# Optimization experiments

Hardware: AMD Instinct MI355X
Metric: run time of the kernel (lower is better)

Reference implementation:

```python
import jax, jax.numpy as jnp
import numpy as np

N = 50000          # num_nodes
E = 800000         # num_edges (avg degree 16)
HID = 128          # hidden_dim
NH = 8             # num_heads
HD = 16            # head_dim
FFN = 512          # ffn_dim
EPS = 1e-5


def setup_inputs() -> dict:
    key = jax.random.key(0)
    ks = jax.random.split(key, 12)
    s = 0.02
    d = {}
    d["x"] = jax.random.normal(ks[0], (N, HID), jnp.float32)
    d["edge_index"] = jax.random.randint(ks[1], (2, E), 0, N, dtype=jnp.int32)
    # projection weights stored as [in, out] (math identical to torch Linear)
    d["Wq"] = jax.random.normal(ks[2], (HID, NH * HD), jnp.float32) * s
    d["bq"] = jnp.zeros((NH * HD,), jnp.float32)
    d["Wk"] = jax.random.normal(ks[3], (HID, NH * HD), jnp.float32) * s
    d["bk"] = jnp.zeros((NH * HD,), jnp.float32)
    d["Wv"] = jax.random.normal(ks[4], (HID, NH * HD), jnp.float32) * s
    d["bv"] = jnp.zeros((NH * HD,), jnp.float32)
    d["Wo"] = jax.random.normal(ks[5], (NH * HD, HID), jnp.float32) * s
    d["bo"] = jnp.zeros((HID,), jnp.float32)
    d["g1"] = jnp.ones((HID,), jnp.float32)
    d["b1"] = jnp.zeros((HID,), jnp.float32)
    d["g2"] = jnp.ones((HID,), jnp.float32)
    d["b2"] = jnp.zeros((HID,), jnp.float32)
    d["W1"] = jax.random.normal(ks[6], (HID, FFN), jnp.float32) * s
    d["bf1"] = jnp.zeros((FFN,), jnp.float32)
    d["W2"] = jax.random.normal(ks[7], (FFN, HID), jnp.float32) * s
    d["bf2"] = jnp.zeros((HID,), jnp.float32)
    return d


def _layer_norm(x, g, b):
    m = jnp.mean(x, axis=-1, keepdims=True)
    v = jnp.mean((x - m) ** 2, axis=-1, keepdims=True)
    return (x - m) * jax.lax.rsqrt(v + EPS) * g + b


def _gnn_layer(x, edge_index, Wq, bq, Wk, bk, Wv, bv, Wo, bo,
               g1, b1, g2, b2, W1, bf1, W2, bf2):
    n = x.shape[0]
    residual = x
    h = _layer_norm(x, g1, b1)

    q = (h @ Wq + bq).reshape(n, NH, HD)
    k = (h @ Wk + bk).reshape(n, NH, HD)
    v = (h @ Wv + bv).reshape(n, NH, HD)

    src, dst = edge_index[0], edge_index[1]
    # original code skips nodes with no in-neighbors (output stays zero)
    deg = jax.ops.segment_sum(jnp.ones(src.shape, x.dtype), dst, num_segments=n)
    # self-loop appended for every attended node
    loops = jnp.arange(n, dtype=src.dtype)
    s_all = jnp.concatenate([src, loops])
    d_all = jnp.concatenate([dst, loops])

    # edge-parallel scaled dot-product scores: [E+N, NH]
    e = jnp.sum(q[d_all] * k[s_all], axis=-1) / np.sqrt(HD).astype(np.float32)
    m = jax.lax.stop_gradient(jax.ops.segment_max(e, d_all, num_segments=n))
    p = jnp.exp(e - m[d_all])
    z = jax.ops.segment_sum(p, d_all, num_segments=n)
    alpha = p / z[d_all]                                   # segment softmax
    agg = jax.ops.segment_sum(alpha[:, :, None] * v[s_all], d_all,
                              num_segments=n)              # [n, NH, HD]
    agg = jnp.where(deg[:, None, None] > 0, agg, jnp.zeros_like(agg))

    att = agg.reshape(n, NH * HD) @ Wo + bo
    x = residual + att                                     # dropout=0 (eval)

    residual = x
    h = _layer_norm(x, g2, b2)
    ffn = jax.nn.gelu(h @ W1 + bf1, approximate=False) @ W2 + bf2
    return residual + ffn


def reference(x, edge_index, Wq, bq, Wk, bk, Wv, bv, Wo, bo,
              g1, b1, g2, b2, W1, bf1, W2, bf2):
    return _gnn_layer(x, edge_index, Wq, bq, Wk, bk, Wv, bv, Wo, bo,
                      g1, b1, g2, b2, W1, bf1, W2, bf2)
```

## Files before the change

kernel.cpp:

```cpp
#include <hip/hip_runtime.h>
#include <hip/hip_bf16.h>

typedef __hip_bfloat16 bf16;
typedef __attribute__((ext_vector_type(8))) short s16x8;
typedef __attribute__((ext_vector_type(4))) float f32x4;

__device__ __forceinline__ float2 bfpair(unsigned u) {
    float2 r;
    r.x = __uint_as_float(u << 16);
    r.y = __uint_as_float(u & 0xffff0000u);
    return r;
}

__device__ __forceinline__ unsigned short f2bf_bits(float f) {
    unsigned u = __float_as_uint(f);
    return (unsigned short)((u + 0x7fffu + ((u >> 16) & 1u)) >> 16);
}

typedef const __attribute__((address_space(1))) unsigned GU;
typedef __attribute__((address_space(3))) unsigned LU;
__device__ __forceinline__ void gload_lds16(const void* g, void* l) {
    __builtin_amdgcn_global_load_lds((GU*)g, (LU*)l, 16, 0, 0);
}

__global__ __launch_bounds__(256) void setup_k(const float* __restrict__ Wq,
                                               const float* __restrict__ Wk,
                                               const float* __restrict__ Wv,
                                               const float* __restrict__ Wo,
                                               const float* __restrict__ W1,
                                               const float* __restrict__ W2,
                                               const float* __restrict__ bq,
                                               const float* __restrict__ bk,
                                               const float* __restrict__ bv,
                                               unsigned short* __restrict__ qkvH,
                                               unsigned short* __restrict__ qkvL,
                                               unsigned short* __restrict__ woH,
                                               unsigned short* __restrict__ woL,
                                               unsigned short* __restrict__ w1H,
                                               unsigned short* __restrict__ w1L,
                                               unsigned short* __restrict__ w2H,
                                               unsigned short* __restrict__ w2L,
                                               float* __restrict__ bqkv,
                                               int* __restrict__ deg,
                                               const unsigned* __restrict__ eisrc,
                                               int* __restrict__ ei32,
                                               int N, int twoE, int nzero) {
    int b = blockIdx.x;
    int tid = threadIdx.x;
    if (b < 770) {
        int idx = b * 256 + tid;
        if (idx >= 196608) {
            int i = idx - 196608;
            if (i < 384) bqkv[i] = (i < 128) ? bq[i] : (i < 256) ? bk[i - 128] : bv[i - 256];
            return;
        }
        float w; unsigned short *H, *L; int oi;
        if (idx < 49152) {
            int n = idx >> 7, kx = idx & 127;
            const float* W = (n < 128) ? Wq : (n < 256) ? Wk : Wv;
            w = W[kx * 128 + (n & 127)];
            H = qkvH; L = qkvL; oi = idx;
        } else if (idx < 65536) {
            int li = idx - 49152; int n = li >> 7, kx = li & 127;
            w = Wo[kx * 128 + n]; H = woH; L = woL; oi = li;
        } else if (idx < 131072) {
            int li = idx - 65536; int n = li >> 7, kx = li & 127;
            w = W1[(size_t)kx * 512 + n]; H = w1H; L = w1L; oi = li;
        } else {
            int li = idx - 131072; int n = li >> 9, kx = li & 511;
            w = W2[(size_t)kx * 128 + n]; H = w2H; L = w2L; oi = li;
        }
        unsigned short hbits = f2bf_bits(w);
        float hf = __uint_as_float((unsigned)hbits << 16);
        H[oi] = hbits;
        L[oi] = f2bf_bits(w - hf);
        return;
    }
    if (b < 770 + nzero) {
        int i = (b - 770) * 256 + tid;
        if (i < N) deg[i] = 0;
        return;
    }
    __shared__ int s_nz;
    if (tid == 0) s_nz = 0;
    __syncthreads();
    if (eisrc[2 * tid + 1] != 0u) atomicAdd(&s_nz, 1);
    __syncthreads();
    bool is64 = (s_nz == 0);
    long long i = (long long)(b - 770 - nzero) * 256 + tid;
    long long st = (long long)2000 * 256;
    if (is64) { for (; i < twoE; i += st) ei32[i] = (int)eisrc[2 * i]; }
    else      { for (; i < twoE; i += st) ei32[i] = (int)eisrc[i]; }
}

__global__ __launch_bounds__(256) void count_deg_k(const int* __restrict__ ei,
                                                   int* __restrict__ deg, int E) {
    int e = blockIdx.x * 256 + threadIdx.x;
    if (e < E) atomicAdd(&deg[ei[E + e]], 1);
}

#define SCAN_BLK 1024
__global__ __launch_bounds__(256) void scan1_k(const int* __restrict__ deg,
                                               int* __restrict__ off,
                                               int* __restrict__ bsum, int n) {
    __shared__ int s[256];
    int base = blockIdx.x * SCAN_BLK;
    int t = threadIdx.x;
    int v[4]; int sum = 0;
    #pragma unroll
    for (int j = 0; j < 4; j++) {
        int idx = base + t * 4 + j;
        v[j] = (idx < n) ? deg[idx] : 0;
        sum += v[j];
    }
    s[t] = sum; __syncthreads();
    for (int o = 1; o < 256; o <<= 1) {
        int add = (t >= o) ? s[t - o] : 0;
        __syncthreads();
        s[t] += add;
        __syncthreads();
    }
    int run = (t > 0) ? s[t - 1] : 0;
    if (t == 255) bsum[blockIdx.x] = s[255];
    #pragma unroll
    for (int j = 0; j < 4; j++) {
        int idx = base + t * 4 + j;
        if (idx < n) off[idx] = run;
        run += v[j];
    }
}

__global__ __launch_bounds__(256) void scan3_k(int* __restrict__ off,
                                               int* __restrict__ cursor,
                                               const int* __restrict__ bsum,
                                               int n, int nb) {
    __shared__ int sb[64];
    int t = threadIdx.x;
    if (t < 64) {
        int own = (t < nb) ? bsum[t] : 0;
        int v = own;
        #pragma unroll
        for (int o = 1; o < 64; o <<= 1) {
            int u = __shfl_up(v, o);
            if ((t & 63) >= o) v += u;
        }
        sb[t] = v - own;
    }
    __syncthreads();
    int i = blockIdx.x * 256 + t;
    if (i < n) {
        int o = off[i] + sb[i / SCAN_BLK];
        off[i] = o;
        cursor[i] = o;
    }
}

__global__ __launch_bounds__(256) void scatter_k(const int* __restrict__ ei,
                                                 int* __restrict__ cursor,
                                                 int* __restrict__ csr, int E) {
    int e = blockIdx.x * 256 + threadIdx.x;
    if (e >= E) return;
    int s = ei[e], d = ei[E + e];
    int pos = atomicAdd(&cursor[d], 1);
    csr[pos] = s;
}

__global__ __launch_bounds__(256) void ln_bf16_k(const float* __restrict__ x,
                                                 const float* __restrict__ g,
                                                 const float* __restrict__ b,
                                                 bf16* __restrict__ out, int M) {
    int row = blockIdx.x * 4 + (threadIdx.x >> 6);
    if (row >= M) return;
    int lane = threadIdx.x & 63;
    float2 f = ((const float2*)x)[(size_t)row * 64 + lane];
    float s = f.x + f.y;
    #pragma unroll
    for (int off = 32; off > 0; off >>= 1) s += __shfl_xor(s, off);
    float mean = s * (1.0f / 128.0f);
    float d0 = f.x - mean, d1 = f.y - mean;
    float vs = d0 * d0 + d1 * d1;
    #pragma unroll
    for (int off = 32; off > 0; off >>= 1) vs += __shfl_xor(vs, off);
    float rstd = rsqrtf(vs * (1.0f / 128.0f) + 1e-5f);
    float2 gg = ((const float2*)g)[lane];
    float2 bb = ((const float2*)b)[lane];
    float o0 = d0 * rstd * gg.x + bb.x;
    float o1 = d1 * rstd * gg.y + bb.y;
    unsigned pk = ((unsigned)f2bf_bits(o1) << 16) | (unsigned)f2bf_bits(o0);
    ((unsigned*)out)[(size_t)row * 64 + lane] = pk;
}

template <int EPI, bool OUTBF, int K, int BM, bool LNF>
__global__ __launch_bounds__(256) void mgemm_k(const bf16* __restrict__ A,
                                               const bf16* __restrict__ Bh,
                                               const bf16* __restrict__ Bl,
                                               const float* __restrict__ bias,
                                               const float* __restrict__ res,
                                               void* __restrict__ outp,
                                               const float* __restrict__ lg,
                                               const float* __restrict__ lb,
                                               bf16* __restrict__ hbout,
                                               long long sub_off, int M,
                                               int ldo, int sub_shift) {
    constexpr int MF = BM / 32;
    constexpr int NK = K / 32;
    constexpr int STEP = BM * 64 + 2 * 8192;
    __shared__ __align__(16) char smem[2 * STEP];

    const int lane = threadIdx.x & 63;
    const int wid  = threadIdx.x >> 6;
    const int wr = wid >> 1, wc = wid & 1;
    const int lrow = lane & 15, lk = lane >> 4;
    const int m0 = blockIdx.y * BM;
    const int mw0 = wr * (BM / 2);
    const int n0 = blockIdx.x * 128 + wc * 64;
    const int srow = lane >> 2;
    const int schunk = (lane & 3) ^ (srow & 3);

    const char* Ab  = (const char*)A  + (size_t)m0 * (K * 2);
    const char* Bhb = (const char*)Bh + (size_t)(blockIdx.x * 128) * (K * 2);
    const char* Blb = (const char*)Bl + (size_t)(blockIdx.x * 128) * (K * 2);

    f32x4 acc[MF][4];
    #pragma unroll
    for (int mf = 0; mf < MF; mf++)
        #pragma unroll
        for (int nf = 0; nf < 4; nf++) {
            f32x4 z = {0.f, 0.f, 0.f, 0.f};
            acc[mf][nf] = z;
        }

    auto stage = [&](int kt, int bufb) {
        const int kb = kt * 64;
        char* sb = &smem[bufb];
        #pragma unroll
        for (int it = 0; it < BM / 64; it++) {
            int rg = wid * (BM / 4) + it * 16;
            gload_lds16(Ab + (size_t)(rg + srow) * (K * 2) + kb + schunk * 16,
                        sb + rg * 64);
        }
        #pragma unroll
        for (int it = 0; it < 2; it++) {
            int rg = wid * 32 + it * 16;
            gload_lds16(Bhb + (size_t)(rg + srow) * (K * 2) + kb + schunk * 16,
                        sb + BM * 64 + rg * 64);
            gload_lds16(Blb + (size_t)(rg + srow) * (K * 2) + kb + schunk * 16,
                        sb + BM * 64 + 8192 + rg * 64);
        }
    };

    auto compute = [&](int bufb) {
        const char* sb = &smem[bufb];
        s16x8 a[MF], bh[4], bl[4];
        #pragma unroll
        for (int mf = 0; mf < MF; mf++) {
            int ra = mw0 + mf * 16 + lrow;
            a[mf] = *(const s16x8*)(sb + ra * 64 + ((lk ^ (ra & 3)) * 16));
        }
        #pragma unroll
        for (int nf = 0; nf < 4; nf++) {
            int rb = wc * 64 + nf * 16 + lrow;
            int co = (lk ^ (rb & 3)) * 16;
            bh[nf] = *(const s16x8*)(sb + BM * 64 + rb * 64 + co);
            bl[nf] = *(const s16x8*)(sb + BM * 64 + 8192 + rb * 64 + co);
        }
        #pragma unroll
        for (int mf = 0; mf < MF; mf++)
            #pragma unroll
            for (int nf = 0; nf < 4; nf++)
                acc[mf][nf] = __builtin_amdgcn_mfma_f32_16x16x32_bf16(a[mf], bh[nf], acc[mf][nf], 0, 0, 0);
        #pragma unroll
        for (int mf = 0; mf < MF; mf++)
            #pragma unroll
            for (int nf = 0; nf < 4; nf++)
                acc[mf][nf] = __builtin_amdgcn_mfma_f32_16x16x32_bf16(a[mf], bl[nf], acc[mf][nf], 0, 0, 0);
    };

    stage(0, 0);
    for (int kt = 0; kt < NK; kt++) {
        __syncthreads();
        if (kt + 1 < NK) stage(kt + 1, ((kt + 1) & 1) * STEP);
        compute((kt & 1) * STEP);
    }

    if (!LNF) {
        const int nmask = (1 << sub_shift) - 1;
        #pragma unroll
        for (int mf = 0; mf < MF; mf++) {
            #pragma unroll
            for (int nf = 0; nf < 4; nf++) {
                int n = n0 + nf * 16 + lrow;
                float bsv = bias[n];
                #pragma unroll
                for (int r = 0; r < 4; r++) {
                    int m = m0 + mw0 + mf * 16 + lk * 4 + r;
                    if (m >= M) continue;
                    float val = acc[mf][nf][r] + bsv;
                    if (EPI == 1) val = 0.5f * val * (1.0f + erff(val * 0.70710678118f));
                    if (EPI == 2) val += res[(size_t)m * ldo + n];
                    long long oidx = (long long)m * ldo + (n & nmask) + (long long)(n >> sub_shift) * sub_off;
                    if (OUTBF) ((unsigned short*)outp)[oidx] = f2bf_bits(val);
                    else       ((float*)outp)[oidx] = val;
                }
            }
        }
    } else {
        float vals[MF][4][4];
        float s1[MF][4], s2[MF][4];
        #pragma unroll
        for (int mf = 0; mf < MF; mf++)
            #pragma unroll
            for (int r = 0; r < 4; r++) { s1[mf][r] = 0.f; s2[mf][r] = 0.f; }
        #pragma unroll
        for (int mf = 0; mf < MF; mf++) {
            #pragma unroll
            for (int r = 0; r < 4; r++) {
                int m = m0 + mw0 + mf * 16 + lk * 4 + r;
                #pragma unroll
                for (int nf = 0; nf < 4; nf++) {
                    int n = n0 + nf * 16 + lrow;
                    float val = acc[mf][nf][r] + bias[n];
                    val += (m < M) ? res[(size_t)m * 128 + n] : 0.f;
                    vals[mf][nf][r] = val;
                    s1[mf][r] += val;
                    s2[mf][r] += val * val;
                }
                #pragma unroll
                for (int o = 1; o < 16; o <<= 1) {
                    s1[mf][r] += __shfl_xor(s1[mf][r], o);
                    s2[mf][r] += __shfl_xor(s2[mf][r], o);
                }
            }
        }
        float2* lns = (float2*)smem;
        __syncthreads();
        if (lrow == 0) {
            #pragma unroll
            for (int mf = 0; mf < MF; mf++)
                #pragma unroll
                for (int r = 0; r < 4; r++) {
                    int rl = mw0 + mf * 16 + lk * 4 + r;
                    float2 p; p.x = s1[mf][r]; p.y = s2[mf][r];
                    lns[rl * 2 + wc] = p;
                }
        }
        __syncthreads();
        #pragma unroll
        for (int mf = 0; mf < MF; mf++) {
            #pragma unroll
            for (int r = 0; r < 4; r++) {
                int rl = mw0 + mf * 16 + lk * 4 + r;
                int m = m0 + rl;
                float2 pa = lns[rl * 2 + 0], pb = lns[rl * 2 + 1];
                float mean = (pa.x + pb.x) * (1.0f / 128.0f);
                float var  = (pa.y + pb.y) * (1.0f / 128.0f) - mean * mean;
                float rstd = rsqrtf(var + 1e-5f);
                if (m >= M) continue;
                #pragma unroll
                for (int nf = 0; nf < 4; nf++) {
                    int n = n0 + nf * 16 + lrow;
                    float val = vals[mf][nf][r];
                    ((float*)outp)[(size_t)m * 128 + n] = val;
                    float o = (val - mean) * rstd * lg[n] + lb[n];
                    ((unsigned short*)hbout)[(size_t)m * 128 + n] = f2bf_bits(o);
                }
            }
        }
    }
}

__global__ __launch_bounds__(256) void node_agg_k(const bf16* __restrict__ q,
                                                  const bf16* __restrict__ k,
                                                  const bf16* __restrict__ v,
                                                  const int* __restrict__ off,
                                                  const int* __restrict__ deg,
                                                  const int* __restrict__ csr,
                                                  bf16* __restrict__ agg, int NN) {
    int node = blockIdx.x * 4 + (threadIdx.x >> 6);
    if (node >= NN) return;
    int lane = threadIdx.x & 63;
    float2 qf = bfpair(((const unsigned*)(q + (size_t)node * 128))[lane]);
    int start = off[node];
    int cnt = deg[node];
    float acc0 = 0.f, acc1 = 0.f, zsum = 0.f;
    if (cnt < 64) {
        int T = cnt + 1;
        int s_vec = (lane < cnt) ? csr[start + lane] : node;
        for (int e0 = 0; e0 < T; e0 += 8) {
            unsigned ku[8], vu[8];
            #pragma unroll
            for (int j = 0; j < 8; j++) {
                if (e0 + j < T) {
                    int s = __shfl(s_vec, e0 + j);
                    ku[j] = ((const unsigned*)(k + (size_t)s * 128))[lane];
                    vu[j] = ((const unsigned*)(v + (size_t)s * 128))[lane];
                }
            }
            #pragma unroll
            for (int j = 0; j < 8; j++) {
                if (e0 + j < T) {
                    float2 kf = bfpair(ku[j]);
                    float dot = qf.x * kf.x + qf.y * kf.y;
                    dot += __shfl_xor(dot, 1);
                    dot += __shfl_xor(dot, 2);
                    dot += __shfl_xor(dot, 4);
                    float p = __expf(dot * 0.25f);
                    zsum += p;
                    float2 vf = bfpair(vu[j]);
                    acc0 += p * vf.x;
                    acc1 += p * vf.y;
                }
            }
        }
    } else {
        for (int e = 0; e <= cnt; e++) {
            int s = (e < cnt) ? csr[start + e] : node;
            float2 kf = bfpair(((const unsigned*)(k + (size_t)s * 128))[lane]);
            float dot = qf.x * kf.x + qf.y * kf.y;
            dot += __shfl_xor(dot, 1);
            dot += __shfl_xor(dot, 2);
            dot += __shfl_xor(dot, 4);
            float p = __expf(dot * 0.25f);
            zsum += p;
            float2 vf = bfpair(((const unsigned*)(v + (size_t)s * 128))[lane]);
            acc0 += p * vf.x;
            acc1 += p * vf.y;
        }
    }
    float2 o;
    if (cnt == 0) { o.x = 0.f; o.y = 0.f; }
    else { float inv = 1.0f / zsum; o.x = acc0 * inv; o.y = acc1 * inv; }
    unsigned pk = ((unsigned)f2bf_bits(o.y) << 16) | (unsigned)f2bf_bits(o.x);
    ((unsigned*)agg)[(size_t)node * 64 + lane] = pk;
}

extern "C" void kernel_launch(void* const* d_in, const int* in_sizes, int n_in,
                              void* d_out, int out_size, void* d_ws, size_t ws_size,
                              hipStream_t stream) {
    const float* x  = (const float*)d_in[0];
    const void*  eiRaw = d_in[1];
    const float* Wq = (const float*)d_in[2];
    const float* bq = (const float*)d_in[3];
    const float* Wk = (const float*)d_in[4];
    const float* bk = (const float*)d_in[5];
    const float* Wv = (const float*)d_in[6];
    const float* bv = (const float*)d_in[7];
    const float* Wo = (const float*)d_in[8];
    const float* bo = (const float*)d_in[9];
    const float* g1 = (const float*)d_in[10];
    const float* b1 = (const float*)d_in[11];
    const float* g2 = (const float*)d_in[12];
    const float* b2 = (const float*)d_in[13];
    const float* W1 = (const float*)d_in[14];
    const float* bf1 = (const float*)d_in[15];
    const float* W2 = (const float*)d_in[16];
    const float* bf2 = (const float*)d_in[17];
    float* out = (float*)d_out;

    const int N = in_sizes[0] / 128;
    const int E = in_sizes[1] / 2;
    const int gy = (N + 127) / 128;
    const int gy64 = (N + 63) / 64;
    const int Mp = gy * 128;

    char* w = (char*)d_ws;
    size_t off_b = 0;
    auto alloc = [&](size_t bytes) -> void* {
        void* ptr = w + off_b;
        off_b = (off_b + bytes + 255) & ~(size_t)255;
        return ptr;
    };
    int*   deg    = (int*)alloc((size_t)N * 4);
    int*   offA   = (int*)alloc((size_t)N * 4);
    int*   cursor = (int*)alloc((size_t)N * 4);
    int*   bsum   = (int*)alloc(64 * 4);
    int*   ei32   = (int*)alloc((size_t)E * 2 * 4);
    int*   csr    = (int*)alloc((size_t)E * 4);
    bf16*  hb     = (bf16*)alloc((size_t)Mp * 128 * 2);
    bf16*  qkvb   = (bf16*)alloc((size_t)N * 3 * 128 * 2);
    bf16*  aggb   = (bf16*)alloc((size_t)Mp * 128 * 2);
    bf16*  t      = (bf16*)alloc((size_t)Mp * 512 * 2);
    unsigned short* qkvH = (unsigned short*)alloc(49152 * 2);
    unsigned short* qkvL = (unsigned short*)alloc(49152 * 2);
    unsigned short* woH  = (unsigned short*)alloc(16384 * 2);
    unsigned short* woL  = (unsigned short*)alloc(16384 * 2);
    unsigned short* w1H  = (unsigned short*)alloc(65536 * 2);
    unsigned short* w1L  = (unsigned short*)alloc(65536 * 2);
    unsigned short* w2H  = (unsigned short*)alloc(65536 * 2);
    unsigned short* w2L  = (unsigned short*)alloc(65536 * 2);
    float* bqkv = (float*)alloc(384 * 4);
    (void)ws_size; (void)n_in; (void)out_size;

    int nb = (N + SCAN_BLK - 1) / SCAN_BLK;
    int nzero = (N + 255) / 256;

    setup_k<<<770 + nzero + 2000, 256, 0, stream>>>(
        Wq, Wk, Wv, Wo, W1, W2, bq, bk, bv,
        qkvH, qkvL, woH, woL, w1H, w1L, w2H, w2L, bqkv,
        deg, (const unsigned*)eiRaw, ei32, N, E * 2, nzero);
    count_deg_k<<<(E + 255) / 256, 256, 0, stream>>>(ei32, deg, E);
    scan1_k<<<nb, 256, 0, stream>>>(deg, offA, bsum, N);
    scan3_k<<<(N + 255) / 256, 256, 0, stream>>>(offA, cursor, bsum, N, nb);
    scatter_k<<<(E + 255) / 256, 256, 0, stream>>>(ei32, cursor, csr, E);

    bf16* qb = qkvb;
    bf16* kb = qkvb + (size_t)N * 128;
    bf16* vb = qkvb + (size_t)N * 256;

    ln_bf16_k<<<(N + 3) / 4, 256, 0, stream>>>(x, g1, b1, hb, N);
    mgemm_k<0, true, 128, 128, false><<<dim3(3, gy), 256, 0, stream>>>(
        hb, (const bf16*)qkvH, (const bf16*)qkvL, bqkv, nullptr, qkvb,
        nullptr, nullptr, nullptr, (long long)N * 128, N, 128, 7);
    node_agg_k<<<(N + 3) / 4, 256, 0, stream>>>(qb, kb, vb, offA, deg, csr, aggb, N);
    mgemm_k<2, false, 128, 64, true><<<dim3(1, gy64), 256, 0, stream>>>(
        aggb, (const bf16*)woH, (const bf16*)woL, bo, x, out,
        g2, b2, hb, 0, N, 128, 15);
    mgemm_k<1, true, 128, 128, false><<<dim3(4, gy), 256, 0, stream>>>(
        hb, (const bf16*)w1H, (const bf16*)w1L, bf1, nullptr, t,
        nullptr, nullptr, nullptr, 0, N, 512, 15);
    mgemm_k<2, false, 512, 64, false><<<dim3(1, gy64), 256, 0, stream>>>(
        t, (const bf16*)w2H, (const bf16*)w2L, bf2, out, out,
        nullptr, nullptr, nullptr, 0, N, 128, 15);
}
```

Measured before the change: 394.8 us.

## Fuse first layernorm into setup kernel, prescale Q, widen agg gather batch

The standalone layernorm kernel becomes extra blocks appended to the setup kernel, which removes one launch and lets that work overlap the setup work. The Q projection epilogue now multiplies Q by 0.25*log2(e), so the aggregation kernel can call raw v_exp_f32 (base-2 exp) without a scale multiply. The aggregation loop also gathers 16 neighbours per batch instead of 8, giving more loads in flight at the cost of more registers. Q is rounded to bf16 after scaling, which slightly changes rounding.

```diff
diff --git a/kernel.cpp b/kernel.cpp
--- a/kernel.cpp
+++ b/kernel.cpp
@@ -22,6 +22,8 @@
 __device__ __forceinline__ void gload_lds16(const void* g, void* l) {
     __builtin_amdgcn_global_load_lds((GU*)g, (LU*)l, 16, 0, 0);
 }
+
+#define QSCALE 0.36067376022f
 
 __global__ __launch_bounds__(256) void setup_k(const float* __restrict__ Wq,
                                                const float* __restrict__ Wk,
@@ -44,6 +46,10 @@
                                                int* __restrict__ deg,
                                                const unsigned* __restrict__ eisrc,
                                                int* __restrict__ ei32,
+                                               const float* __restrict__ x,
+                                               const float* __restrict__ g1,
+                                               const float* __restrict__ b1,
+                                               bf16* __restrict__ hb,
                                                int N, int twoE, int nzero) {
     int b = blockIdx.x;
     int tid = threadIdx.x;
@@ -81,16 +87,38 @@
         if (i < N) deg[i] = 0;
         return;
     }
-    __shared__ int s_nz;
-    if (tid == 0) s_nz = 0;
-    __syncthreads();
-    if (eisrc[2 * tid + 1] != 0u) atomicAdd(&s_nz, 1);
-    __syncthreads();
-    bool is64 = (s_nz == 0);
-    long long i = (long long)(b - 770 - nzero) * 256 + tid;
-    long long st = (long long)2000 * 256;
-    if (is64) { for (; i < twoE; i += st) ei32[i] = (int)eisrc[2 * i]; }
-    else      { for (; i < twoE; i += st) ei32[i] = (int)eisrc[i]; }
+    if (b < 770 + nzero + 2000) {
+        __shared__ int s_nz;
+        if (tid == 0) s_nz = 0;
+        __syncthreads();
+        if (eisrc[2 * tid + 1] != 0u) atomicAdd(&s_nz, 1);
+        __syncthreads();
+        bool is64 = (s_nz == 0);
+        long long i = (long long)(b - 770 - nzero) * 256 + tid;
+        long long st = (long long)2000 * 256;
+        if (is64) { for (; i < twoE; i += st) ei32[i] = (int)eisrc[2 * i]; }
+        else      { for (; i < twoE; i += st) ei32[i] = (int)eisrc[i]; }
+        return;
+    }
+    int row = (b - 770 - nzero - 2000) * 4 + (tid >> 6);
+    if (row >= N) return;
+    int lane = tid & 63;
+    float2 f = ((const float2*)x)[(size_t)row * 64 + lane];
+    float s = f.x + f.y;
+    #pragma unroll
+    for (int off = 32; off > 0; off >>= 1) s += __shfl_xor(s, off);
+    float mean = s * (1.0f / 128.0f);
+    float d0 = f.x - mean, d1 = f.y - mean;
+    float vs = d0 * d0 + d1 * d1;
+    #pragma unroll
+    for (int off = 32; off > 0; off >>= 1) vs += __shfl_xor(vs, off);
+    float rstd = rsqrtf(vs * (1.0f / 128.0f) + 1e-5f);
+    float2 gg = ((const float2*)g1)[lane];
+    float2 bb = ((const float2*)b1)[lane];
+    float o0 = d0 * rstd * gg.x + bb.x;
+    float o1 = d1 * rstd * gg.y + bb.y;
+    unsigned pk = ((unsigned)f2bf_bits(o1) << 16) | (unsigned)f2bf_bits(o0);
+    ((unsigned*)hb)[(size_t)row * 64 + lane] = pk;
 }
 
 __global__ __launch_bounds__(256) void count_deg_k(const int* __restrict__ ei,
@@ -165,32 +193,7 @@
     csr[pos] = s;
 }
 
-__global__ __launch_bounds__(256) void ln_bf16_k(const float* __restrict__ x,
-                                                 const float* __restrict__ g,
-                                                 const float* __restrict__ b,
-                                                 bf16* __restrict__ out, int M) {
-    int row = blockIdx.x * 4 + (threadIdx.x >> 6);
-    if (row >= M) return;
-    int lane = threadIdx.x & 63;
-    float2 f = ((const float2*)x)[(size_t)row * 64 + lane];
-    float s = f.x + f.y;
-    #pragma unroll
-    for (int off = 32; off > 0; off >>= 1) s += __shfl_xor(s, off);
-    float mean = s * (1.0f / 128.0f);
-    float d0 = f.x - mean, d1 = f.y - mean;
-    float vs = d0 * d0 + d1 * d1;
-    #pragma unroll
-    for (int off = 32; off > 0; off >>= 1) vs += __shfl_xor(vs, off);
-    float rstd = rsqrtf(vs * (1.0f / 128.0f) + 1e-5f);
-    float2 gg = ((const float2*)g)[lane];
-    float2 bb = ((const float2*)b)[lane];
-    float o0 = d0 * rstd * gg.x + bb.x;
-    float o1 = d1 * rstd * gg.y + bb.y;
-    unsigned pk = ((unsigned)f2bf_bits(o1) << 16) | (unsigned)f2bf_bits(o0);
-    ((unsigned*)out)[(size_t)row * 64 + lane] = pk;
-}
-
-template <int EPI, bool OUTBF, int K, int BM, bool LNF>
+template <int EPI, bool OUTBF, int K, int BM, bool LNF, bool QS>
 __global__ __launch_bounds__(256) void mgemm_k(const bf16* __restrict__ A,
                                                const bf16* __restrict__ Bh,
                                                const bf16* __restrict__ Bl,
@@ -298,6 +301,7 @@
                     float val = acc[mf][nf][r] + bsv;
                     if (EPI == 1) val = 0.5f * val * (1.0f + erff(val * 0.70710678118f));
                     if (EPI == 2) val += res[(size_t)m * ldo + n];
+                    if (QS && n < 128) val *= QSCALE;
                     long long oidx = (long long)m * ldo + (n & nmask) + (long long)(n >> sub_shift) * sub_off;
                     if (OUTBF) ((unsigned short*)outp)[oidx] = f2bf_bits(val);
                     else       ((float*)outp)[oidx] = val;
@@ -386,10 +390,10 @@
     if (cnt < 64) {
         int T = cnt + 1;
         int s_vec = (lane < cnt) ? csr[start + lane] : node;
-        for (int e0 = 0; e0 < T; e0 += 8) {
-            unsigned ku[8], vu[8];
-            #pragma unroll
-            for (int j = 0; j < 8; j++) {
+        for (int e0 = 0; e0 < T; e0 += 16) {
+            unsigned ku[16], vu[16];
+            #pragma unroll
+            for (int j = 0; j < 16; j++) {
                 if (e0 + j < T) {
                     int s = __shfl(s_vec, e0 + j);
                     ku[j] = ((const unsigned*)(k + (size_t)s * 128))[lane];
@@ -397,14 +401,15 @@
                 }
             }
             #pragma unroll
-            for (int j = 0; j < 8; j++) {
+            for (int j = 0; j < 16; j++) {
                 if (e0 + j < T) {
                     float2 kf = bfpair(ku[j]);
                     float dot = qf.x * kf.x + qf.y * kf.y;
                     dot += __shfl_xor(dot, 1);
                     dot += __shfl_xor(dot, 2);
                     dot += __shfl_xor(dot, 4);
-                    float p = __expf(dot * 0.25f);
+                    float p;
+                    asm("v_exp_f32 %0, %1" : "=v"(p) : "v"(dot));
                     zsum += p;
                     float2 vf = bfpair(vu[j]);
                     acc0 += p * vf.x;
@@ -420,7 +425,8 @@
             dot += __shfl_xor(dot, 1);
             dot += __shfl_xor(dot, 2);
             dot += __shfl_xor(dot, 4);
-            float p = __expf(dot * 0.25f);
+            float p;
+            asm("v_exp_f32 %0, %1" : "=v"(p) : "v"(dot));
             zsum += p;
             float2 vf = bfpair(((const unsigned*)(v + (size_t)s * 128))[lane]);
             acc0 += p * vf.x;
@@ -493,11 +499,12 @@
 
     int nb = (N + SCAN_BLK - 1) / SCAN_BLK;
     int nzero = (N + 255) / 256;
-
-    setup_k<<<770 + nzero + 2000, 256, 0, stream>>>(
+    int lnb = (N + 3) / 4;
+
+    setup_k<<<770 + nzero + 2000 + lnb, 256, 0, stream>>>(
         Wq, Wk, Wv, Wo, W1, W2, bq, bk, bv,
         qkvH, qkvL, woH, woL, w1H, w1L, w2H, w2L, bqkv,
-        deg, (const unsigned*)eiRaw, ei32, N, E * 2, nzero);
+        deg, (const unsigned*)eiRaw, ei32, x, g1, b1, hb, N, E * 2, nzero);
     count_deg_k<<<(E + 255) / 256, 256, 0, stream>>>(ei32, deg, E);
     scan1_k<<<nb, 256, 0, stream>>>(deg, offA, bsum, N);
     scan3_k<<<(N + 255) / 256, 256, 0, stream>>>(offA, cursor, bsum, N, nb);
@@ -507,18 +514,17 @@
     bf16* kb = qkvb + (size_t)N * 128;
     bf16* vb = qkvb + (size_t)N * 256;
 
-    ln_bf16_k<<<(N + 3) / 4, 256, 0, stream>>>(x, g1, b1, hb, N);
-    mgemm_k<0, true, 128, 128, false><<<dim3(3, gy), 256, 0, stream>>>(
+    mgemm_k<0, true, 128, 128, false, true><<<dim3(3, gy), 256, 0, stream>>>(
         hb, (const bf16*)qkvH, (const bf16*)qkvL, bqkv, nullptr, qkvb,
         nullptr, nullptr, nullptr, (long long)N * 128, N, 128, 7);
     node_agg_k<<<(N + 3) / 4, 256, 0, stream>>>(qb, kb, vb, offA, deg, csr, aggb, N);
-    mgemm_k<2, false, 128, 64, true><<<dim3(1, gy64), 256, 0, stream>>>(
+    mgemm_k<2, false, 128, 64, true, false><<<dim3(1, gy64), 256, 0, stream>>>(
         aggb, (const bf16*)woH, (const bf16*)woL, bo, x, out,
         g2, b2, hb, 0, N, 128, 15);
-    mgemm_k<1, true, 128, 128, false><<<dim3(4, gy), 256, 0, stream>>>(
+    mgemm_k<1, true, 128, 128, false, false><<<dim3(4, gy), 256, 0, stream>>>(
         hb, (const bf16*)w1H, (const bf16*)w1L, bf1, nullptr, t,
         nullptr, nullptr, nullptr, 0, N, 512, 15);
-    mgemm_k<2, false, 512, 64, false><<<dim3(1, gy64), 256, 0, stream>>>(
+    mgemm_k<2, false, 512, 64, false, false><<<dim3(1, gy64), 256, 0, stream>>>(
         t, (const bf16*)w2H, (const bf16*)w2L, bf2, out, out,
         nullptr, nullptr, nullptr, 0, N, 128, 15);
 }
```

Result: slower. 443.0 us (+12.2%).
